# Performance work log

Measured on AMD Instinct MI355X. Metric: run time of the kernel, lower is better.

The kernel has to match this reference:

```python
import jax, jax.numpy as jnp
import numpy as np

B = 16
D_MODEL = 1024
HALF = D_MODEL // 2
PATTERN_NUM = 4096
PATTERN_LEN = 32          # == patch_seq_len
ENC_SEQ = 2048
SIM_NUM = 64
NUM_PATCH = ENC_SEQ // PATTERN_LEN


def setup_inputs() -> dict:
    key = jax.random.key(0)
    ks = jax.random.split(key, 6)
    w = lambda k, shape: jax.random.normal(k, shape, jnp.float32) * 0.02
    return {
        "src": jax.random.normal(ks[0], (B, ENC_SEQ, D_MODEL), jnp.float32),
        "meta_pattern_pool": jax.random.normal(ks[1], (PATTERN_NUM, PATTERN_LEN), jnp.float32),
        "fuse_w": w(ks[2], (PATTERN_LEN * HALF, SIM_NUM)),
        "fuse_b": jnp.zeros((SIM_NUM,), jnp.float32),
        "recover_w": w(ks[3], (SIM_NUM, HALF)),
        "recover_b": jnp.zeros((HALF,), jnp.float32),
        "gp_w": w(ks[4], (HALF, 10)),
        "gp_b": jnp.zeros((10,), jnp.float32),
    }


def reference(src, meta_pattern_pool, fuse_w, fuse_b, recover_w, recover_b, gp_w, gp_b):
    # src: [B, S, D]; take second half of channels and split into patches
    x = src[:, :, HALF:].reshape(B, NUM_PATCH, PATTERN_LEN, HALF)  # [B,P,L,H]

    # per-patch similarity score against pattern pool (vectorized over patches)
    low = jnp.mean(x @ gp_w + gp_b, axis=-1)                       # [B,P,L]
    scores = jnp.einsum('bpl,nl->bpn', low, meta_pattern_pool)     # [B,P,N]

    # topk pattern retrieval; original uses batch-0 indices for all batches
    _, idx = jax.lax.top_k(scores, SIM_NUM)                        # [B,P,S]
    selected = meta_pattern_pool[idx[0]]                           # [P,S,L]

    # softmax routing key per patch
    logits = x.reshape(B, NUM_PATCH, PATTERN_LEN * HALF) @ fuse_w + fuse_b
    route = jax.nn.softmax(logits, axis=-1)                        # [B,P,S]

    # fuse[b,p,l,s] = route[b,p,s] * selected[p,s,l]
    fuse = route[:, :, None, :] * jnp.transpose(selected, (0, 2, 1))[None]  # [B,P,L,S]
    out = (fuse @ recover_w + recover_b).reshape(B, ENC_SEQ, HALF)

    padding = jnp.einsum('bps,psl->bpl', route, selected).reshape(B, ENC_SEQ)

    out_full = jnp.concatenate([src[:, :, :HALF], out], axis=-1)   # [B,S,D]
    # original prepends an uninitialized torch.empty buffer; we use zeros
    padding_out = jnp.concatenate([jnp.zeros((B, ENC_SEQ), src.dtype), padding], axis=-1)
    return out_full, padding_out
```

## Files before the change

kernel.cpp:

```cpp
#include <hip/hip_runtime.h>
#include <hip/hip_bf16.h>

#define NB 16
#define DMODEL 1024
#define HALFD 512
#define PNUM 4096
#define PLEN 32
#define SEQ 2048
#define SIM 64
#define NPATCH 64
#define NROWS (NB*SEQ)
#define MROWS (NB*NPATCH)
#define KDIM (PLEN*HALFD)
#define NCOPY 512
#define OUT0 ((size_t)NB*SEQ*DMODEL)

typedef __attribute__((ext_vector_type(8))) short s8v;
typedef __attribute__((ext_vector_type(4))) float f32x4;
typedef __attribute__((ext_vector_type(8))) unsigned short ush8;
typedef unsigned long long u64;

__device__ __forceinline__ unsigned short f2bf(float f) {
    __hip_bfloat16 h = __float2bfloat16(f);
    return *reinterpret_cast<unsigned short*>(&h);
}
__device__ __forceinline__ float bf2f(unsigned short u) {
    __hip_bfloat16 h = *reinterpret_cast<__hip_bfloat16*>(&u);
    return __bfloat162float(h);
}
__device__ __forceinline__ u64 umax64(u64 a, u64 b) { return a > b ? a : b; }
__device__ __forceinline__ u64 umin64(u64 a, u64 b) { return a < b ? a : b; }
__device__ __forceinline__ u64 clean6(u64 v, int lane) {
    #pragma unroll
    for (int j = 32; j; j >>= 1) {
        u64 o = __shfl_xor(v, j);
        v = ((lane & j) == 0) ? umax64(v, o) : umin64(v, o);
    }
    return v;
}

union PrepShared {
    float tile[64][68];
    double gpm[513];
};
__global__ __launch_bounds__(256) void k_prep(
        const float* __restrict__ gp_w, const float* __restrict__ gp_b,
        const float* __restrict__ fw, const float* __restrict__ rw,
        const float* __restrict__ src,
        unsigned short* __restrict__ fwT_hi, unsigned short* __restrict__ fwT_lo,
        unsigned short* __restrict__ rwf_hi, unsigned short* __restrict__ rwf_lo,
        double* __restrict__ low) {
    __shared__ PrepShared u;
    int bid = blockIdx.x, t = threadIdx.x;
    if (bid < 256) {
        int k0 = bid * 64;
        int i = t >> 2;
        #pragma unroll
        for (int q = 0; q < 4; ++q) {
            int c = (t & 3) + q*4;
            float4 v = *reinterpret_cast<const float4*>(fw + (size_t)(k0 + i)*SIM + c*4);
            *reinterpret_cast<float4*>(&u.tile[i][c*4]) = v;
        }
        __syncthreads();
        #pragma unroll
        for (int c2 = 0; c2 < 2; ++c2) {
            int e = c2*256 + t;
            int kl = e >> 8, fn = (e >> 6) & 3, l = e & 63;
            int kk0 = kl*32 + ((l >> 4) * 8), n = fn*16 + (l & 15);
            ush8 hv, lv;
            #pragma unroll
            for (int j = 0; j < 8; ++j) {
                float f = u.tile[kk0 + j][n];
                unsigned short hb = f2bf(f);
                hv[j] = hb;
                lv[j] = f2bf(f - bf2f(hb));
            }
            size_t dst = ((size_t)((2*bid + kl)*4 + fn)*64 + l)*8;
            *reinterpret_cast<ush8*>(fwT_hi + dst) = hv;
            *reinterpret_cast<ush8*>(fwT_lo + dst) = lv;
        }
    } else if (bid < 768) {
        for (int h = t; h < HALFD; h += 256) {
            double s = 0.0;
            #pragma unroll
            for (int j = 0; j < 10; ++j) s += (double)gp_w[h*10 + j];
            u.gpm[h] = s / 10.0;
        }
        if (t == 0) {
            double sb = 0.0;
            #pragma unroll
            for (int j = 0; j < 10; ++j) sb += (double)gp_b[j];
            u.gpm[512] = sb / 10.0;
        }
        __syncthreads();
        int r = (bid - 256)*4 + (t >> 6);
        int lane = t & 63;
        const float4* s4 = reinterpret_cast<const float4*>(src + (size_t)r * DMODEL);
        float4 x0 = s4[128 + lane];
        float4 x1 = s4[192 + lane];
        const double* g0 = u.gpm + lane*4;
        const double* g1 = u.gpm + 256 + lane*4;
        double d = (double)x0.x*g0[0] + (double)x0.y*g0[1] + (double)x0.z*g0[2] + (double)x0.w*g0[3]
                 + (double)x1.x*g1[0] + (double)x1.y*g1[1] + (double)x1.z*g1[2] + (double)x1.w*g1[3];
        #pragma unroll
        for (int o = 32; o; o >>= 1) d += __shfl_xor(d, o);
        if (lane == 0) low[r] = d + u.gpm[512];
    } else {
        int lane = t & 63, q = t >> 6;
        int idx = (bid - 768)*4 + q;
        int ks = idx >> 5, fn = idx & 31;
        int ml = lane & 15, kg = lane >> 4;
        ush8 hv, lv;
        #pragma unroll
        for (int j = 0; j < 8; ++j) {
            float f = rw[(size_t)(ks*32 + kg*8 + j)*HALFD + fn*16 + ml];
            unsigned short hb = f2bf(f);
            hv[j] = hb;
            lv[j] = f2bf(f - bf2f(hb));
        }
        size_t dst = ((size_t)idx*64 + lane)*8;
        *reinterpret_cast<ush8*>(rwf_hi + dst) = hv;
        *reinterpret_cast<ush8*>(rwf_lo + dst) = lv;
    }
}

__global__ __launch_bounds__(256) void k_topk(
        const double* __restrict__ low, const float* __restrict__ pool,
        u64* __restrict__ cand) {
    __shared__ double lowp[PLEN];
    __shared__ u64 wl[4][64];
    int t = threadIdx.x, lane = t & 63, w = t >> 6;
    int p = blockIdx.x >> 3, q = blockIdx.x & 7;
    if (t < PLEN) lowp[t] = low[p*PLEN + t];
    __syncthreads();
    u64 v[2];
    #pragma unroll
    for (int cc = 0; cc < 2; ++cc) {
        int n = q*512 + (w*2 + cc)*64 + lane;
        const float4* p4 = reinterpret_cast<const float4*>(pool + (size_t)n*PLEN);
        double s = 0.0;
        #pragma unroll
        for (int r2 = 0; r2 < 8; ++r2) {
            float4 vv = p4[r2];
            s += (double)vv.x*lowp[r2*4] + (double)vv.y*lowp[r2*4+1]
               + (double)vv.z*lowp[r2*4+2] + (double)vv.w*lowp[r2*4+3];
        }
        u64 ub = (u64)__double_as_longlong(s);
        u64 okey = ub ^ (((u64)((long long)ub >> 63)) | 0x8000000000000000ULL);
        v[cc] = (okey & ~0xFFFULL) | (u64)(0xFFF - n);
    }
    #pragma unroll
    for (int kk = 2; kk <= 64; kk <<= 1) {
        #pragma unroll
        for (int j = kk >> 1; j; j >>= 1) {
            #pragma unroll
            for (int cc = 0; cc < 2; ++cc) {
                u64 o = __shfl_xor(v[cc], j);
                bool keepMax = ((lane & kk) == 0) == ((lane & j) == 0);
                v[cc] = keepMax ? umax64(v[cc], o) : umin64(v[cc], o);
            }
        }
    }
    u64 rb2 = __shfl(v[1], 63 - lane);
    u64 m = umax64(v[0], rb2);
    m = clean6(m, lane);
    wl[w][lane] = m;
    __syncthreads();
    if (w == 0) {
        u64 a = umax64(wl[0][lane], wl[1][63 - lane]); a = clean6(a, lane);
        u64 b = umax64(wl[2][lane], wl[3][63 - lane]); b = clean6(b, lane);
        u64 r2 = __shfl(b, 63 - lane);
        u64 f = umax64(a, r2); f = clean6(f, lane);
        cand[(size_t)(p*8 + q)*SIM + lane] = f;
    }
}

__global__ __launch_bounds__(256) void k_logits(
        const float* __restrict__ src,
        const unsigned short* __restrict__ fwT_hi, const unsigned short* __restrict__ fwT_lo,
        float* __restrict__ part, float* __restrict__ out, int nks) {
    int t = threadIdx.x, lane = t & 63, w = t >> 6;
    if ((int)blockIdx.x >= 16*nks) {
        int cb = blockIdx.x - 16*nks;
        size_t total = (size_t)NROWS * 128;
        const float4* s4 = reinterpret_cast<const float4*>(src);
        float4* o4 = reinterpret_cast<float4*>(out);
        for (size_t idx = (size_t)cb*256 + t; idx < total; idx += (size_t)NCOPY*256) {
            size_t r = idx >> 7, c = idx & 127;
            o4[r*256 + c] = s4[r*256 + c];
        }
        return;
    }
    int mt = blockIdx.x / nks, ks = blockIdx.x - mt*nks;
    int kchunk = KDIM / nks, nstep = kchunk >> 6;
    int r0 = mt*64;
    int ml = lane & 15, kg = lane >> 4;
    int Rrow = r0 + w*16 + ml;
    int bb = Rrow >> 6, prow = Rrow & 63;
    const float* xrow = src + ((size_t)(bb*SEQ + prow*PLEN))*DMODEL + HALFD;
    int kblk_base = (ks*kchunk) >> 5;
    f32x4 acc[4] = {};
    for (int step = 0; step < nstep; ++step) {
        int k0 = ks*kchunk + step*64;
        int l = k0 >> 9, h0 = k0 & 511;
        const float* ap = xrow + (size_t)l*DMODEL + h0 + kg*8;
        float4 va0 = *reinterpret_cast<const float4*>(ap);
        float4 va1 = *reinterpret_cast<const float4*>(ap + 4);
        float4 vb0 = *reinterpret_cast<const float4*>(ap + 32);
        float4 vb1 = *reinterpret_cast<const float4*>(ap + 36);
        s8v ah0, al0, ah1, al1;
        float fa[8] = {va0.x,va0.y,va0.z,va0.w,va1.x,va1.y,va1.z,va1.w};
        float fbv[8] = {vb0.x,vb0.y,vb0.z,vb0.w,vb1.x,vb1.y,vb1.z,vb1.w};
        #pragma unroll
        for (int j = 0; j < 8; ++j) {
            unsigned short hb = f2bf(fa[j]);
            ah0[j] = (short)hb;
            al0[j] = (short)f2bf(fa[j] - bf2f(hb));
            unsigned short hb2 = f2bf(fbv[j]);
            ah1[j] = (short)hb2;
            al1[j] = (short)f2bf(fbv[j] - bf2f(hb2));
        }
        int kblk0 = kblk_base + step*2;
        #pragma unroll
        for (int fn = 0; fn < 4; ++fn) {
            size_t off0 = ((size_t)(kblk0*4 + fn)*64 + lane)*8;
            size_t off1 = ((size_t)((kblk0+1)*4 + fn)*64 + lane)*8;
            s8v bh0 = *reinterpret_cast<const s8v*>(fwT_hi + off0);
            s8v bl0 = *reinterpret_cast<const s8v*>(fwT_lo + off0);
            s8v bh1 = *reinterpret_cast<const s8v*>(fwT_hi + off1);
            s8v bl1 = *reinterpret_cast<const s8v*>(fwT_lo + off1);
            acc[fn] = __builtin_amdgcn_mfma_f32_16x16x32_bf16(ah0, bh0, acc[fn], 0, 0, 0);
            acc[fn] = __builtin_amdgcn_mfma_f32_16x16x32_bf16(ah0, bl0, acc[fn], 0, 0, 0);
            acc[fn] = __builtin_amdgcn_mfma_f32_16x16x32_bf16(al0, bh0, acc[fn], 0, 0, 0);
            acc[fn] = __builtin_amdgcn_mfma_f32_16x16x32_bf16(ah1, bh1, acc[fn], 0, 0, 0);
            acc[fn] = __builtin_amdgcn_mfma_f32_16x16x32_bf16(ah1, bl1, acc[fn], 0, 0, 0);
            acc[fn] = __builtin_amdgcn_mfma_f32_16x16x32_bf16(al1, bh1, acc[fn], 0, 0, 0);
        }
    }
    float* pout = part + (size_t)(mt*nks + ks)*4096;
    #pragma unroll
    for (int fn = 0; fn < 4; ++fn)
        #pragma unroll
        for (int r = 0; r < 4; ++r)
            pout[(w*16 + kg*4 + r)*64 + fn*16 + ml] = acc[fn][r];
}

__global__ __launch_bounds__(256) void k_out(
        const float* __restrict__ part, const float* __restrict__ fb,
        const u64* __restrict__ cand, const float* __restrict__ pool,
        const unsigned short* __restrict__ rwf_hi, const unsigned short* __restrict__ rwf_lo,
        const float* __restrict__ rb, float* __restrict__ out,
        float* __restrict__ pad, int nks) {
    __shared__ float A_T[SIM][36];
    __shared__ float routeS[64];
    __shared__ int   selS[64];
    __shared__ float psum[4][64];
    int row = blockIdx.x;
    int b = row >> 6, p = row & 63;
    int t = threadIdx.x, lane = t & 63, w = t >> 6;
    int kpw = nks >> 2;
    {
        float v = 0.f;
        for (int kq = 0; kq < kpw; ++kq) {
            int ks = w*kpw + kq;
            v += part[(size_t)(b*nks + ks)*4096 + p*64 + lane];
        }
        psum[w][lane] = v;
    }
    __syncthreads();
    if (w == 0) {
        float v = psum[0][lane] + psum[1][lane] + psum[2][lane] + psum[3][lane] + fb[lane];
        float m = v;
        #pragma unroll
        for (int o = 32; o; o >>= 1) m = fmaxf(m, __shfl_xor(m, o));
        float e = expf(v - m);
        float sum = e;
        #pragma unroll
        for (int o = 32; o; o >>= 1) sum += __shfl_xor(sum, o);
        routeS[lane] = e / sum;
    } else if (w == 1) {
        const u64* c = cand + (size_t)p*8*SIM;
        u64 a = umax64(c[lane],         c[1*SIM + 63 - lane]); a = clean6(a, lane);
        u64 bq = umax64(c[2*SIM + lane], c[3*SIM + 63 - lane]); bq = clean6(bq, lane);
        u64 d = umax64(c[4*SIM + lane], c[5*SIM + 63 - lane]); d = clean6(d, lane);
        u64 e = umax64(c[6*SIM + lane], c[7*SIM + 63 - lane]); e = clean6(e, lane);
        u64 ab = umax64(a, __shfl(bq, 63 - lane)); ab = clean6(ab, lane);
        u64 de = umax64(d, __shfl(e, 63 - lane)); de = clean6(de, lane);
        u64 f  = umax64(ab, __shfl(de, 63 - lane)); f = clean6(f, lane);
        selS[lane] = 0xFFF - (int)(f & 0xFFFULL);
    }
    __syncthreads();
    #pragma unroll
    for (int q = 0; q < 8; ++q) {
        int e = t + q*256;
        int s = e >> 5, l = e & 31;
        A_T[s][l] = routeS[s] * pool[(size_t)selS[s]*PLEN + l];
    }
    __syncthreads();
    if (t < 32) {
        float ps = 0.f;
        #pragma unroll
        for (int s = 0; s < 64; ++s) ps += A_T[s][t];
        pad[(size_t)b*2*SEQ + SEQ + p*PLEN + t] = ps;
    } else if (t < 64) {
        pad[(size_t)b*2*SEQ + p*PLEN + (t - 32)] = 0.f;
    }
    int ml = lane & 15, kg = lane >> 4;
    s8v ah[2][2], al[2][2];
    #pragma unroll
    for (int mt = 0; mt < 2; ++mt)
        #pragma unroll
        for (int ks = 0; ks < 2; ++ks) {
            #pragma unroll
            for (int j = 0; j < 8; ++j) {
                float f = A_T[ks*32 + kg*8 + j][mt*16 + ml];
                unsigned short hb = f2bf(f);
                ah[mt][ks][j] = (short)hb;
                al[mt][ks][j] = (short)f2bf(f - bf2f(hb));
            }
        }
    size_t orow0 = ((size_t)(b*SEQ + p*PLEN))*DMODEL + HALFD;
    #pragma unroll
    for (int nt = 0; nt < 8; ++nt) {
        int fng = w*8 + nt;
        f32x4 acc0 = {}, acc1 = {};
        #pragma unroll
        for (int ks = 0; ks < 2; ++ks) {
            size_t off = ((size_t)(ks*32 + fng)*64 + lane)*8;
            s8v bh = *reinterpret_cast<const s8v*>(rwf_hi + off);
            s8v bl = *reinterpret_cast<const s8v*>(rwf_lo + off);
            acc0 = __builtin_amdgcn_mfma_f32_16x16x32_bf16(ah[0][ks], bh, acc0, 0, 0, 0);
            acc0 = __builtin_amdgcn_mfma_f32_16x16x32_bf16(ah[0][ks], bl, acc0, 0, 0, 0);
            acc0 = __builtin_amdgcn_mfma_f32_16x16x32_bf16(al[0][ks], bh, acc0, 0, 0, 0);
            acc1 = __builtin_amdgcn_mfma_f32_16x16x32_bf16(ah[1][ks], bh, acc1, 0, 0, 0);
            acc1 = __builtin_amdgcn_mfma_f32_16x16x32_bf16(ah[1][ks], bl, acc1, 0, 0, 0);
            acc1 = __builtin_amdgcn_mfma_f32_16x16x32_bf16(al[1][ks], bh, acc1, 0, 0, 0);
        }
        int n = fng*16 + ml;
        float bias = rb[n];
        #pragma unroll
        for (int r = 0; r < 4; ++r) {
            int m0 = kg*4 + r;
            out[orow0 + (size_t)m0*DMODEL + n]        = acc0[r] + bias;
            out[orow0 + (size_t)(16 + m0)*DMODEL + n] = acc1[r] + bias;
        }
    }
}

static const void* by_size(void* const* d_in, const int* in_sizes, int n_in,
                           int want, int fallback) {
    for (int i = 0; i < n_in; ++i) if (in_sizes[i] == want) return d_in[i];
    return d_in[fallback];
}

extern "C" void kernel_launch(void* const* d_in, const int* in_sizes, int n_in,
                              void* d_out, int out_size, void* d_ws, size_t ws_size,
                              hipStream_t stream) {
    const float* src  = (const float*)by_size(d_in, in_sizes, n_in, NB*SEQ*DMODEL, 0);
    const float* pool = (const float*)by_size(d_in, in_sizes, n_in, PNUM*PLEN, 1);
    const float* fw   = (const float*)by_size(d_in, in_sizes, n_in, KDIM*SIM, 2);
    const float* fb   = (const float*)by_size(d_in, in_sizes, n_in, SIM, 3);
    const float* rw   = (const float*)by_size(d_in, in_sizes, n_in, SIM*HALFD, 4);
    const float* rb   = (const float*)by_size(d_in, in_sizes, n_in, HALFD, 5);
    const float* gpw  = (const float*)by_size(d_in, in_sizes, n_in, HALFD*10, 6);
    const float* gpb  = (const float*)by_size(d_in, in_sizes, n_in, 10, 7);
    float* out = (float*)d_out;
    float* pad = out + OUT0;

    int nks = (ws_size >= (size_t)(16u << 20)) ? 32 : 8;

    unsigned short* fwT_hi = (unsigned short*)d_ws;
    unsigned short* fwT_lo = fwT_hi + (size_t)SIM*KDIM;
    unsigned short* rwf_hi = fwT_lo + (size_t)SIM*KDIM;
    unsigned short* rwf_lo = rwf_hi + (size_t)SIM*HALFD;
    double* low  = (double*)(rwf_lo + (size_t)SIM*HALFD);
    u64*   cand  = (u64*)(low + 2048);
    float* part  = (float*)(cand + (size_t)NPATCH*8*SIM);

    hipLaunchKernelGGL(k_prep,   dim3(784),    dim3(256), 0, stream,
                       gpw, gpb, fw, rw, src, fwT_hi, fwT_lo, rwf_hi, rwf_lo, low);
    hipLaunchKernelGGL(k_topk,   dim3(512),    dim3(256), 0, stream, low, pool, cand);
    hipLaunchKernelGGL(k_logits, dim3(16*nks + NCOPY), dim3(256), 0, stream,
                       src, fwT_hi, fwT_lo, part, out, nks);
    hipLaunchKernelGGL(k_out,    dim3(MROWS),  dim3(256), 0, stream,
                       part, fb, cand, pool, rwf_hi, rwf_lo, rb, out, pad, nks);
}
```

Baseline: 101.7 us.

## Fuse top-k scoring into prep kernel and remap block indices for XCD locality

Folds the separate top-k kernel into the prep kernel. Each of 512 blocks now computes the low-rank projection for its patch's 32 rows, then scores and sorts its slice of the pattern pool, which removes one launch and the round trip of `low` through global memory. The trade-off is that each patch's 32 rows of src and the gp_w mean are recomputed eight times, once per q-block. It also remaps block IDs in k_logits and k_out so that consecutive blocks (bid & 7), which the scheduler spreads across chiplets, are grouped for better L2 locality.

```diff
diff --git a/kernel.cpp b/kernel.cpp
--- a/kernel.cpp
+++ b/kernel.cpp
@@ -40,20 +40,92 @@
 }
 
 union PrepShared {
+    struct { double gpm[513]; double lowp[PLEN]; u64 wl[4][64]; } tk;
     float tile[64][68];
-    double gpm[513];
 };
 __global__ __launch_bounds__(256) void k_prep(
         const float* __restrict__ gp_w, const float* __restrict__ gp_b,
         const float* __restrict__ fw, const float* __restrict__ rw,
-        const float* __restrict__ src,
+        const float* __restrict__ src, const float* __restrict__ pool,
         unsigned short* __restrict__ fwT_hi, unsigned short* __restrict__ fwT_lo,
         unsigned short* __restrict__ rwf_hi, unsigned short* __restrict__ rwf_lo,
-        double* __restrict__ low) {
+        u64* __restrict__ cand) {
     __shared__ PrepShared u;
     int bid = blockIdx.x, t = threadIdx.x;
-    if (bid < 256) {
-        int k0 = bid * 64;
+    int lane = t & 63, w = t >> 6;
+    if (bid < 512) {
+        int p = bid >> 3, q = bid & 7;
+        for (int h = t; h < HALFD; h += 256) {
+            double s = 0.0;
+            #pragma unroll
+            for (int j = 0; j < 10; ++j) s += (double)gp_w[h*10 + j];
+            u.tk.gpm[h] = s / 10.0;
+        }
+        if (t == 0) {
+            double sb = 0.0;
+            #pragma unroll
+            for (int j = 0; j < 10; ++j) sb += (double)gp_b[j];
+            u.tk.gpm[512] = sb / 10.0;
+        }
+        __syncthreads();
+        {
+            const double* g0 = u.tk.gpm + lane*4;
+            const double* g1 = u.tk.gpm + 256 + lane*4;
+            #pragma unroll
+            for (int rr = 0; rr < 8; ++rr) {
+                int r = w*8 + rr;
+                const float4* s4 = reinterpret_cast<const float4*>(src + (size_t)(p*PLEN + r)*DMODEL);
+                float4 x0 = s4[128 + lane], x1 = s4[192 + lane];
+                double d = (double)x0.x*g0[0] + (double)x0.y*g0[1] + (double)x0.z*g0[2] + (double)x0.w*g0[3]
+                         + (double)x1.x*g1[0] + (double)x1.y*g1[1] + (double)x1.z*g1[2] + (double)x1.w*g1[3];
+                #pragma unroll
+                for (int o = 32; o; o >>= 1) d += __shfl_xor(d, o);
+                if (lane == 0) u.tk.lowp[r] = d + u.tk.gpm[512];
+            }
+        }
+        __syncthreads();
+        u64 v[2];
+        #pragma unroll
+        for (int cc = 0; cc < 2; ++cc) {
+            int n = q*512 + (w*2 + cc)*64 + lane;
+            const float4* p4 = reinterpret_cast<const float4*>(pool + (size_t)n*PLEN);
+            double s = 0.0;
+            #pragma unroll
+            for (int r2 = 0; r2 < 8; ++r2) {
+                float4 vv = p4[r2];
+                s += (double)vv.x*u.tk.lowp[r2*4] + (double)vv.y*u.tk.lowp[r2*4+1]
+                   + (double)vv.z*u.tk.lowp[r2*4+2] + (double)vv.w*u.tk.lowp[r2*4+3];
+            }
+            u64 ub = (u64)__double_as_longlong(s);
+            u64 okey = ub ^ (((u64)((long long)ub >> 63)) | 0x8000000000000000ULL);
+            v[cc] = (okey & ~0xFFFULL) | (u64)(0xFFF - n);
+        }
+        #pragma unroll
+        for (int kk = 2; kk <= 64; kk <<= 1) {
+            #pragma unroll
+            for (int j = kk >> 1; j; j >>= 1) {
+                #pragma unroll
+                for (int cc = 0; cc < 2; ++cc) {
+                    u64 o = __shfl_xor(v[cc], j);
+                    bool keepMax = ((lane & kk) == 0) == ((lane & j) == 0);
+                    v[cc] = keepMax ? umax64(v[cc], o) : umin64(v[cc], o);
+                }
+            }
+        }
+        u64 rb2 = __shfl(v[1], 63 - lane);
+        u64 m = umax64(v[0], rb2);
+        m = clean6(m, lane);
+        u.tk.wl[w][lane] = m;
+        __syncthreads();
+        if (w == 0) {
+            u64 a = umax64(u.tk.wl[0][lane], u.tk.wl[1][63 - lane]); a = clean6(a, lane);
+            u64 b = umax64(u.tk.wl[2][lane], u.tk.wl[3][63 - lane]); b = clean6(b, lane);
+            u64 r2 = __shfl(b, 63 - lane);
+            u64 f = umax64(a, r2); f = clean6(f, lane);
+            cand[(size_t)(p*8 + q)*SIM + lane] = f;
+        }
+    } else if (bid < 768) {
+        int k0 = (bid - 512) * 64;
         int i = t >> 2;
         #pragma unroll
         for (int q = 0; q < 4; ++q) {
@@ -75,38 +147,12 @@
                 hv[j] = hb;
                 lv[j] = f2bf(f - bf2f(hb));
             }
-            size_t dst = ((size_t)((2*bid + kl)*4 + fn)*64 + l)*8;
+            size_t dst = ((size_t)((2*(bid - 512) + kl)*4 + fn)*64 + l)*8;
             *reinterpret_cast<ush8*>(fwT_hi + dst) = hv;
             *reinterpret_cast<ush8*>(fwT_lo + dst) = lv;
         }
-    } else if (bid < 768) {
-        for (int h = t; h < HALFD; h += 256) {
-            double s = 0.0;
-            #pragma unroll
-            for (int j = 0; j < 10; ++j) s += (double)gp_w[h*10 + j];
-            u.gpm[h] = s / 10.0;
-        }
-        if (t == 0) {
-            double sb = 0.0;
-            #pragma unroll
-            for (int j = 0; j < 10; ++j) sb += (double)gp_b[j];
-            u.gpm[512] = sb / 10.0;
-        }
-        __syncthreads();
-        int r = (bid - 256)*4 + (t >> 6);
-        int lane = t & 63;
-        const float4* s4 = reinterpret_cast<const float4*>(src + (size_t)r * DMODEL);
-        float4 x0 = s4[128 + lane];
-        float4 x1 = s4[192 + lane];
-        const double* g0 = u.gpm + lane*4;
-        const double* g1 = u.gpm + 256 + lane*4;
-        double d = (double)x0.x*g0[0] + (double)x0.y*g0[1] + (double)x0.z*g0[2] + (double)x0.w*g0[3]
-                 + (double)x1.x*g1[0] + (double)x1.y*g1[1] + (double)x1.z*g1[2] + (double)x1.w*g1[3];
-        #pragma unroll
-        for (int o = 32; o; o >>= 1) d += __shfl_xor(d, o);
-        if (lane == 0) low[r] = d + u.gpm[512];
     } else {
-        int lane = t & 63, q = t >> 6;
+        int q = t >> 6;
         int idx = (bid - 768)*4 + q;
         int ks = idx >> 5, fn = idx & 31;
         int ml = lane & 15, kg = lane >> 4;
@@ -124,64 +170,14 @@
     }
 }
 
-__global__ __launch_bounds__(256) void k_topk(
-        const double* __restrict__ low, const float* __restrict__ pool,
-        u64* __restrict__ cand) {
-    __shared__ double lowp[PLEN];
-    __shared__ u64 wl[4][64];
-    int t = threadIdx.x, lane = t & 63, w = t >> 6;
-    int p = blockIdx.x >> 3, q = blockIdx.x & 7;
-    if (t < PLEN) lowp[t] = low[p*PLEN + t];
-    __syncthreads();
-    u64 v[2];
-    #pragma unroll
-    for (int cc = 0; cc < 2; ++cc) {
-        int n = q*512 + (w*2 + cc)*64 + lane;
-        const float4* p4 = reinterpret_cast<const float4*>(pool + (size_t)n*PLEN);
-        double s = 0.0;
-        #pragma unroll
-        for (int r2 = 0; r2 < 8; ++r2) {
-            float4 vv = p4[r2];
-            s += (double)vv.x*lowp[r2*4] + (double)vv.y*lowp[r2*4+1]
-               + (double)vv.z*lowp[r2*4+2] + (double)vv.w*lowp[r2*4+3];
-        }
-        u64 ub = (u64)__double_as_longlong(s);
-        u64 okey = ub ^ (((u64)((long long)ub >> 63)) | 0x8000000000000000ULL);
-        v[cc] = (okey & ~0xFFFULL) | (u64)(0xFFF - n);
-    }
-    #pragma unroll
-    for (int kk = 2; kk <= 64; kk <<= 1) {
-        #pragma unroll
-        for (int j = kk >> 1; j; j >>= 1) {
-            #pragma unroll
-            for (int cc = 0; cc < 2; ++cc) {
-                u64 o = __shfl_xor(v[cc], j);
-                bool keepMax = ((lane & kk) == 0) == ((lane & j) == 0);
-                v[cc] = keepMax ? umax64(v[cc], o) : umin64(v[cc], o);
-            }
-        }
-    }
-    u64 rb2 = __shfl(v[1], 63 - lane);
-    u64 m = umax64(v[0], rb2);
-    m = clean6(m, lane);
-    wl[w][lane] = m;
-    __syncthreads();
-    if (w == 0) {
-        u64 a = umax64(wl[0][lane], wl[1][63 - lane]); a = clean6(a, lane);
-        u64 b = umax64(wl[2][lane], wl[3][63 - lane]); b = clean6(b, lane);
-        u64 r2 = __shfl(b, 63 - lane);
-        u64 f = umax64(a, r2); f = clean6(f, lane);
-        cand[(size_t)(p*8 + q)*SIM + lane] = f;
-    }
-}
-
 __global__ __launch_bounds__(256) void k_logits(
         const float* __restrict__ src,
         const unsigned short* __restrict__ fwT_hi, const unsigned short* __restrict__ fwT_lo,
         float* __restrict__ part, float* __restrict__ out, int nks) {
     int t = threadIdx.x, lane = t & 63, w = t >> 6;
-    if ((int)blockIdx.x >= 16*nks) {
-        int cb = blockIdx.x - 16*nks;
+    int bid = blockIdx.x;
+    if (bid >= 16*nks) {
+        int cb = bid - 16*nks;
         size_t total = (size_t)NROWS * 128;
         const float4* s4 = reinterpret_cast<const float4*>(src);
         float4* o4 = reinterpret_cast<float4*>(out);
@@ -191,7 +187,8 @@
         }
         return;
     }
-    int mt = blockIdx.x / nks, ks = blockIdx.x - mt*nks;
+    int g = (bid & 7)*(2*nks) + (bid >> 3);
+    int mt = g / nks, ks = g - mt*nks;
     int kchunk = KDIM / nks, nstep = kchunk >> 6;
     int r0 = mt*64;
     int ml = lane & 15, kg = lane >> 4;
@@ -255,7 +252,7 @@
     __shared__ float routeS[64];
     __shared__ int   selS[64];
     __shared__ float psum[4][64];
-    int row = blockIdx.x;
+    int row = (blockIdx.x & 7)*(MROWS/8) + (blockIdx.x >> 3);
     int b = row >> 6, p = row & 63;
     int t = threadIdx.x, lane = t & 63, w = t >> 6;
     int kpw = nks >> 2;
@@ -373,13 +370,11 @@
     unsigned short* fwT_lo = fwT_hi + (size_t)SIM*KDIM;
     unsigned short* rwf_hi = fwT_lo + (size_t)SIM*KDIM;
     unsigned short* rwf_lo = rwf_hi + (size_t)SIM*HALFD;
-    double* low  = (double*)(rwf_lo + (size_t)SIM*HALFD);
-    u64*   cand  = (u64*)(low + 2048);
+    u64*   cand  = (u64*)(rwf_lo + (size_t)SIM*HALFD);
     float* part  = (float*)(cand + (size_t)NPATCH*8*SIM);
 
     hipLaunchKernelGGL(k_prep,   dim3(784),    dim3(256), 0, stream,
-                       gpw, gpb, fw, rw, src, fwT_hi, fwT_lo, rwf_hi, rwf_lo, low);
-    hipLaunchKernelGGL(k_topk,   dim3(512),    dim3(256), 0, stream, low, pool, cand);
+                       gpw, gpb, fw, rw, src, pool, fwT_hi, fwT_lo, rwf_hi, rwf_lo, cand);
     hipLaunchKernelGGL(k_logits, dim3(16*nks + NCOPY), dim3(256), 0, stream,
                        src, fwT_hi, fwT_lo, part, out, nks);
     hipLaunchKernelGGL(k_out,    dim3(MROWS),  dim3(256), 0, stream,
```

Result: no change. 101.5 us (-0.3%).
